# Performance work log

Hardware: AMD Instinct MI355X
Metric: run time of the kernel (lower is better)

Reference implementation:

```python
import jax, jax.numpy as jnp
import numpy as np

NUM_NODES = 100000
NUM_RELATIONS = 8
EMB_DIM = 128
HIDDEN_L = 64
NUM_LABELS = 32
NUM_EDGES = 1600000


def setup_inputs() -> dict:
    key = jax.random.key(0)
    ks = jax.random.split(key, 9)
    edge_index = jax.random.randint(ks[0], (2, NUM_EDGES), 0, NUM_NODES, dtype=jnp.int64)
    edge_type = jax.random.randint(ks[1], (NUM_EDGES,), 0, NUM_RELATIONS, dtype=jnp.int64)
    embedding = jax.random.normal(ks[2], (NUM_NODES, EMB_DIM), dtype=jnp.float32)
    W1 = jax.random.normal(ks[3], (NUM_RELATIONS, EMB_DIM, HIDDEN_L), dtype=jnp.float32) * (1.0 / np.sqrt(EMB_DIM))
    root1 = jax.random.normal(ks[4], (EMB_DIM, HIDDEN_L), dtype=jnp.float32) * (1.0 / np.sqrt(EMB_DIM))
    bias1 = jnp.zeros((HIDDEN_L,), dtype=jnp.float32)
    W2 = jax.random.normal(ks[5], (NUM_RELATIONS, HIDDEN_L, NUM_LABELS), dtype=jnp.float32) * (1.0 / np.sqrt(HIDDEN_L))
    root2 = jax.random.normal(ks[6], (HIDDEN_L, NUM_LABELS), dtype=jnp.float32) * (1.0 / np.sqrt(HIDDEN_L))
    bias2 = jnp.zeros((NUM_LABELS,), dtype=jnp.float32)
    return {"edge_index": edge_index, "edge_type": edge_type, "embedding": embedding,
            "W1": W1, "root1": root1, "bias1": bias1, "W2": W2, "root2": root2, "bias2": bias2}


def _rgcn_conv(x, edge_index, edge_type, W, root, bias):
    # PyG RGCNConv (default): out = bias + x @ root + sum_r mean_{j in N_r(i)} (x_j @ W_r)
    # Mean commutes with the linear map, so aggregate x_j per (dst, relation) first,
    # then apply the relation weights with one grouped einsum.
    n, r = x.shape[0], W.shape[0]
    src, dst = edge_index[0], edge_index[1]
    seg = dst * r + edge_type  # composite segment id: (node, relation)
    sums = jax.ops.segment_sum(x[src], seg, num_segments=n * r)          # [N*R, F_in]
    counts = jax.ops.segment_sum(jnp.ones_like(seg, dtype=x.dtype), seg, num_segments=n * r)
    mean = sums / jnp.maximum(counts, 1.0)[:, None]                      # [N*R, F_in]
    mean = mean.reshape(n, r, -1)                                        # [N, R, F_in]
    out = jnp.einsum('nrf,rfo->no', mean, W) + x @ root + bias           # [N, F_out]
    return out


def reference(edge_index, edge_type, embedding, W1, root1, bias1, W2, root2, bias2):
    x = _rgcn_conv(embedding, edge_index, edge_type, W1, root1, bias1)
    x = jax.nn.relu(x)
    x = _rgcn_conv(x, edge_index, edge_type, W2, root2, bias2)
    return jax.nn.sigmoid(x)
```

## Files before the change

kernel.cpp:

```cpp
#include <hip/hip_runtime.h>
#include <cstdint>

#define RR 8
#define D0 128
#define D1 64
#define D2 32
#define BINSH 8
#define EPB 4096

typedef unsigned short u16;
typedef unsigned int u32;
typedef short short8 __attribute__((ext_vector_type(8)));
typedef float floatx4 __attribute__((ext_vector_type(4)));

static __device__ __forceinline__ float relu_f(float x) { return x > 0.f ? x : 0.f; }
static __device__ __forceinline__ float sigm_f(float x) { return 1.0f / (1.0f + __expf(-x)); }

static __device__ __forceinline__ u16 f2bf(float x) {
  unsigned int u = __float_as_uint(x);
  u += 0x7fffu + ((u >> 16) & 1u);
  return (u16)(u >> 16);
}
static __device__ __forceinline__ float bf2f(u16 v) {
  return __uint_as_float(((unsigned int)v) << 16);
}

static __device__ __forceinline__ void packBTf_body(
    const float* __restrict__ W, const float* __restrict__ root,
    u16* __restrict__ BTf, int K, int NKf, int FOUT, int NC, int YC, int i) {
  if (i >= NC * K) return;
  int j = i & 7, l = (i >> 3) & 63, rest = i >> 9;
  int ks = rest % NKf, ct = rest / NKf;
  int c = ct * 16 + (l & 15);
  int k = ks * 32 + (l >> 4) * 8 + j;
  float v;
  if (c < YC) { int r = c / FOUT, o = c - r * FOUT; v = W[((size_t)r * K + k) * FOUT + o]; }
  else        { int o = c - YC; v = root[(size_t)k * (NC - YC) + o]; }
  BTf[i] = f2bf(v);
}

__global__ __launch_bounds__(256) void prep_k(
    const int* __restrict__ dstp, int E,
    const float* __restrict__ W1, const float* __restrict__ root1, u16* __restrict__ BT1,
    const float* __restrict__ W2, const float* __restrict__ root2, u16* __restrict__ BT2,
    int* __restrict__ histg, int NBIN, int NBLK, int nbBinA, int nbP1) {
  int b = blockIdx.x;
  if (b < nbBinA) {
    __shared__ int hist[512];
    int blk = b, t = threadIdx.x;
    for (int i = t; i < NBIN; i += 256) hist[i] = 0;
    __syncthreads();
    int base = blk * EPB + t;
#pragma unroll
    for (int j = 0; j < 16; ++j) {
      int e = base + j * 256;
      if (e < E) atomicAdd(&hist[dstp[e] >> BINSH], 1);
    }
    __syncthreads();
    for (int i = t; i < NBIN; i += 256) histg[(size_t)i * NBLK + blk] = hist[i];
  } else if (b < nbBinA + nbP1) {
    packBTf_body(W1, root1, BT1, D0, D0 / 32, D1, RR * D1 + D1, RR * D1,
                 (b - nbBinA) * 256 + threadIdx.x);
  } else {
    packBTf_body(W2, root2, BT2, D1, D1 / 32, D2, RR * D2 + D2, RR * D2,
                 (b - nbBinA - nbP1) * 256 + threadIdx.x);
  }
}

__global__ __launch_bounds__(256) void hsum_k(
    const int* __restrict__ histg, int* __restrict__ hbsum, int hl) {
  __shared__ int sd[256];
  int b = blockIdx.x, t = threadIdx.x;
  int base = b * 1024 + t * 4;
  int s = 0;
#pragma unroll
  for (int j = 0; j < 4; ++j) { int i = base + j; if (i < hl) s += histg[i]; }
  sd[t] = s; __syncthreads();
  for (int st = 128; st > 0; st >>= 1) { if (t < st) sd[t] += sd[t + st]; __syncthreads(); }
  if (t == 0) hbsum[b] = sd[0];
}

__global__ void hscan2_k(int* __restrict__ hbsum, int nb) {
  __shared__ int sd[256];
  int t = threadIdx.x;
  int v = (t < nb) ? hbsum[t] : 0;
  sd[t] = v; __syncthreads();
  for (int st = 1; st < 256; st <<= 1) {
    int x = (t >= st) ? sd[t - st] : 0;
    __syncthreads(); sd[t] += x; __syncthreads();
  }
  if (t < nb) hbsum[t] = sd[t] - v;
}

__global__ void hscan3_k(const int* __restrict__ histg, const int* __restrict__ hbsum,
                         int* __restrict__ hscan, int hl) {
  __shared__ int sd[256];
  int blk = blockIdx.x, t = threadIdx.x;
  int base = blk * 1024 + t * 4;
  int vals[4]; int s = 0; int loc[4];
#pragma unroll
  for (int j = 0; j < 4; ++j) {
    int i = base + j; int x = (i < hl) ? histg[i] : 0;
    vals[j] = x; loc[j] = s; s += x;
  }
  sd[t] = s; __syncthreads();
  for (int st = 1; st < 256; st <<= 1) {
    int x = (t >= st) ? sd[t - st] : 0;
    __syncthreads(); sd[t] += x; __syncthreads();
  }
  int texcl = sd[t] - s;
#pragma unroll
  for (int j = 0; j < 4; ++j) {
    int i = base + j;
    if (i < hl) {
      hscan[i] = hbsum[blk] + texcl + loc[j];
      if (i == hl - 1) hscan[hl] = hbsum[blk] + texcl + loc[j] + vals[j];
    }
  }
}

__global__ __launch_bounds__(256) void binB_k(
    const int* __restrict__ src, const int* __restrict__ dstp, const int* __restrict__ et,
    const int* __restrict__ hscan, int2* __restrict__ pk, int NBIN, int NBLK, int E) {
  __shared__ int curB[512];
  int blk = blockIdx.x, t = threadIdx.x;
  for (int i = t; i < NBIN; i += 256) curB[i] = hscan[(size_t)i * NBLK + blk];
  __syncthreads();
  int base = blk * EPB + t;
#pragma unroll
  for (int j = 0; j < 16; ++j) {
    int e = base + j * 256;
    if (e < E) {
      int d = dstp[e];
      int pos = atomicAdd(&curB[d >> BINSH], 1);
      pk[pos] = make_int2(src[e] * RR + et[e], d);
    }
  }
}

template <int K, int NC, int YC, bool AF32>
static __device__ __forceinline__ void gemm_body(
    const void* __restrict__ Aptr, const u16* __restrict__ BTf,
    const float* __restrict__ bias, u16* __restrict__ Y,
    float* __restrict__ Xroot, int N, int rowBlk, u16* __restrict__ smem) {
  constexpr int KP = K + 8;
  constexpr int NK = K / 32;
  constexpr int NCT = NC / 16;
  constexpr int ROOTC = NC - YC;
  constexpr int CH = K / 8;
  constexpr int YTS = 72;
  u16* const Al = smem;
  const int tid = threadIdx.x;

  if (AF32) {
    const float* A = (const float*)Aptr;
    for (int c = tid; c < 64 * CH; c += 256) {
      int row = c / CH, kc = c - row * CH;
      int gr = rowBlk * 64 + row; if (gr >= N) gr = N - 1;
      const float4* p = (const float4*)&A[(size_t)gr * K + kc * 8];
      float4 v0 = p[0], v1 = p[1];
      uint4 o;
      o.x = (u32)f2bf(v0.x) | ((u32)f2bf(v0.y) << 16);
      o.y = (u32)f2bf(v0.z) | ((u32)f2bf(v0.w) << 16);
      o.z = (u32)f2bf(v1.x) | ((u32)f2bf(v1.y) << 16);
      o.w = (u32)f2bf(v1.z) | ((u32)f2bf(v1.w) << 16);
      *(uint4*)&Al[row * KP + kc * 8] = o;
    }
  } else {
    const u16* A = (const u16*)Aptr;
    for (int c = tid; c < 64 * CH; c += 256) {
      int row = c / CH, kc = c - row * CH;
      int gr = rowBlk * 64 + row; if (gr >= N) gr = N - 1;
      *(uint4*)&Al[row * KP + kc * 8] = *(const uint4*)&A[(size_t)gr * K + kc * 8];
    }
  }
  __syncthreads();

  const int lane = tid & 63, wid = tid >> 6;
  const int l16 = lane & 15, quad = lane >> 4;
  const int wrow = (wid >> 1) * 32, wcol = (wid & 1) * 32;

  short8 af[2][NK];
#pragma unroll
  for (int ks = 0; ks < NK; ++ks) {
    int ko = ks * 32 + quad * 8;
    af[0][ks] = *(const short8*)&Al[(wrow +      l16) * KP + ko];
    af[1][ks] = *(const short8*)&Al[(wrow + 16 + l16) * KP + ko];
  }
  __syncthreads();

  int p = 0;
#pragma unroll
  for (int cb = 0; cb < NC; cb += 64, ++p) {
    int ct0 = (cb + wcol) >> 4; if (ct0 > NCT - 1) ct0 = NCT - 1;
    int ct1 = ct0 + 1;          if (ct1 > NCT - 1) ct1 = NCT - 1;

    short8 bf0[NK], bf1[NK];
#pragma unroll
    for (int ks = 0; ks < NK; ++ks) {
      bf0[ks] = *(const short8*)&BTf[((size_t)(ct0 * NK + ks) * 64 + lane) * 8];
      bf1[ks] = *(const short8*)&BTf[((size_t)(ct1 * NK + ks) * 64 + lane) * 8];
    }

    floatx4 acc[2][2] = {};
#pragma unroll
    for (int ks = 0; ks < NK; ++ks) {
      acc[0][0] = __builtin_amdgcn_mfma_f32_16x16x32_bf16(bf0[ks], af[0][ks], acc[0][0], 0, 0, 0);
      acc[0][1] = __builtin_amdgcn_mfma_f32_16x16x32_bf16(bf1[ks], af[0][ks], acc[0][1], 0, 0, 0);
      acc[1][0] = __builtin_amdgcn_mfma_f32_16x16x32_bf16(bf0[ks], af[1][ks], acc[1][0], 0, 0, 0);
      acc[1][1] = __builtin_amdgcn_mfma_f32_16x16x32_bf16(bf1[ks], af[1][ks], acc[1][1], 0, 0, 0);
    }

    if (cb + 64 <= YC) {
      u16* yt = smem + (p & 1) * (64 * YTS);
#pragma unroll
      for (int mi = 0; mi < 2; ++mi)
#pragma unroll
        for (int ni = 0; ni < 2; ++ni) {
          floatx4 v = acc[mi][ni];
          uint2 o;
          o.x = (u32)f2bf(v[0]) | ((u32)f2bf(v[1]) << 16);
          o.y = (u32)f2bf(v[2]) | ((u32)f2bf(v[3]) << 16);
          *(uint2*)&yt[(wrow + mi * 16 + l16) * YTS + wcol + ni * 16 + quad * 4] = o;
        }
    } else {
#pragma unroll
      for (int mi = 0; mi < 2; ++mi) {
        int r = rowBlk * 64 + wrow + mi * 16 + l16;
        if (r >= N) continue;
#pragma unroll
        for (int ni = 0; ni < 2; ++ni) {
          int cbase = cb + wcol + ni * 16 + quad * 4;
          floatx4 v = acc[mi][ni];
          if (cbase >= YC && cbase < NC) {
            int o = cbase - YC;
            float4 w;
            w.x = v[0] + bias[o];     w.y = v[1] + bias[o + 1];
            w.z = v[2] + bias[o + 2]; w.w = v[3] + bias[o + 3];
            *(float4*)&Xroot[(size_t)r * ROOTC + o] = w;
          }
        }
      }
    }
    __syncthreads();
    if (cb + 64 <= YC) {
      const u16* yt = smem + (p & 1) * (64 * YTS);
#pragma unroll
      for (int u = tid; u < 512; u += 256) {
        int row = u >> 3, cg = u & 7;
        int gr = rowBlk * 64 + row;
        if (gr < N)
          *(uint4*)&Y[(size_t)gr * YC + cb + cg * 8] = *(const uint4*)&yt[row * YTS + cg * 8];
      }
    }
  }
}

template <int K, int NC, int YC, bool AF32>
__global__ __launch_bounds__(256) void gemm_k(
    const void* __restrict__ Aptr, const u16* __restrict__ BTf,
    const float* __restrict__ bias, u16* __restrict__ Y,
    float* __restrict__ Xroot, int N) {
  constexpr int AL_U16 = 64 * (K + 8);
  constexpr int YT_U16 = 2 * 64 * 72;
  constexpr int SM_U16 = AL_U16 > YT_U16 ? AL_U16 : YT_U16;
  __shared__ __align__(16) u16 smem[SM_U16];
  gemm_body<K, NC, YC, AF32>(Aptr, BTf, bias, Y, Xroot, N, blockIdx.x, smem);
}

__global__ __launch_bounds__(256) void pgB2_k(
    const void* __restrict__ emb, const u16* __restrict__ BT1, const float* __restrict__ b1,
    u16* __restrict__ Y, float* __restrict__ xr1, int N, int nbBinC,
    const int2* __restrict__ pk, const int* __restrict__ hscan,
    int* __restrict__ offs, float* __restrict__ invc, int* __restrict__ ssr,
    int NBIN, int NBLK, int E) {
  constexpr int AL_U16 = 64 * (D0 + 8);
  constexpr int YT_U16 = 2 * 64 * 72;
  constexpr int SM_U16 = AL_U16 > YT_U16 ? AL_U16 : YT_U16;
  __shared__ __align__(16) u16 smem[SM_U16];
  if ((int)blockIdx.x >= nbBinC) {
    gemm_body<D0, RR * D1 + D1, RR * D1, true>(emb, BT1, b1, Y, xr1, N,
                                               blockIdx.x - nbBinC, smem);
    return;
  }
  int* cnt  = (int*)smem;
  int* tot  = cnt + 2048;
  int* sd   = tot + 256;
  int* curL = sd + 256;
  int b = blockIdx.x, t = threadIdx.x;
  int beg = hscan[(size_t)b * NBLK];
  int end = hscan[(size_t)(b + 1) * NBLK];
  int node0 = b << BINSH;

  for (int i = t; i < 2048; i += 256) cnt[i] = 0;
  __syncthreads();
  for (int i = beg + t; i < end; i += 256) {
    int2 p = pk[i];
    atomicAdd(&cnt[((p.y - node0) << 3) + (p.x & 7)], 1);
  }
  __syncthreads();

  int d = node0 + t;
  int s = 0;
  float iv[RR];
#pragma unroll
  for (int r = 0; r < RR; ++r) {
    int c = cnt[(t << 3) + r];
    s += c;
    iv[r] = 1.0f / (float)(c > 1 ? c : 1);
  }
  if (d < N) {
#pragma unroll
    for (int r = 0; r < RR; ++r) invc[(size_t)d * RR + r] = iv[r];
  }
  sd[t] = s; __syncthreads();
  for (int st = 1; st < 256; st <<= 1) {
    int x = (t >= st) ? sd[t - st] : 0;
    __syncthreads(); sd[t] += x; __syncthreads();
  }
  int excl = sd[t] - s;
  tot[t] = excl;
  if (d < N) offs[d] = beg + excl;
  if (d == N - 1) offs[N] = beg + excl + s;
  curL[t] = 0;
  __syncthreads();

  for (int i = beg + t; i < end; i += 256) {
    int2 p = pk[i];
    int ln = p.y - node0;
    int r = atomicAdd(&curL[ln], 1);
    ssr[beg + tot[ln] + r] = p.x;
  }
}

__global__ __launch_bounds__(256) void agg1_k(
    const int* __restrict__ off, const int* __restrict__ ssr,
    const uint4* __restrict__ Yu, const float* __restrict__ invc,
    const float4* __restrict__ xroot, uint4* __restrict__ X1b, int N, int E) {
  int d = blockIdx.x * 4 + (threadIdx.x >> 6);
  if (d >= N) return;
  int lane = threadIdx.x & 63;
  int h = lane >> 3, fi = lane & 7;
  int beg = off[d], end = off[d + 1];
  int deg = end - beg;
  int ei = beg + lane; if (ei >= E) ei = E - 1;
  int e = ssr[ei];
  float a0 = 0.f, a1 = 0.f, a2 = 0.f, a3 = 0.f, a4 = 0.f, a5 = 0.f, a6 = 0.f, a7 = 0.f;
  int dcap = deg < 64 ? deg : 64;
  for (int jb = 0; jb < dcap; jb += 16) {
    int j0 = jb + h, j1 = jb + 8 + h;
    int sr0 = __shfl(e, j0);
    int sr1 = __shfl(e, j1);
    if (j0 < deg) {
      float w = invc[(d << 3) + (sr0 & 7)];
      uint4 y = Yu[(size_t)sr0 * 8 + fi];
      a0 = fmaf(bf2f((u16)y.x), w, a0); a1 = fmaf(bf2f((u16)(y.x >> 16)), w, a1);
      a2 = fmaf(bf2f((u16)y.y), w, a2); a3 = fmaf(bf2f((u16)(y.y >> 16)), w, a3);
      a4 = fmaf(bf2f((u16)y.z), w, a4); a5 = fmaf(bf2f((u16)(y.z >> 16)), w, a5);
      a6 = fmaf(bf2f((u16)y.w), w, a6); a7 = fmaf(bf2f((u16)(y.w >> 16)), w, a7);
    }
    if (j1 < deg) {
      float w = invc[(d << 3) + (sr1 & 7)];
      uint4 y = Yu[(size_t)sr1 * 8 + fi];
      a0 = fmaf(bf2f((u16)y.x), w, a0); a1 = fmaf(bf2f((u16)(y.x >> 16)), w, a1);
      a2 = fmaf(bf2f((u16)y.y), w, a2); a3 = fmaf(bf2f((u16)(y.y >> 16)), w, a3);
      a4 = fmaf(bf2f((u16)y.z), w, a4); a5 = fmaf(bf2f((u16)(y.z >> 16)), w, a5);
      a6 = fmaf(bf2f((u16)y.w), w, a6); a7 = fmaf(bf2f((u16)(y.w >> 16)), w, a7);
    }
  }
  if (deg > 64) {
    for (int i = beg + 64 + h; i < end; i += 8) {
      int sr = ssr[i];
      float w = invc[(d << 3) + (sr & 7)];
      uint4 y = Yu[(size_t)sr * 8 + fi];
      a0 = fmaf(bf2f((u16)y.x), w, a0); a1 = fmaf(bf2f((u16)(y.x >> 16)), w, a1);
      a2 = fmaf(bf2f((u16)y.y), w, a2); a3 = fmaf(bf2f((u16)(y.y >> 16)), w, a3);
      a4 = fmaf(bf2f((u16)y.z), w, a4); a5 = fmaf(bf2f((u16)(y.z >> 16)), w, a5);
      a6 = fmaf(bf2f((u16)y.w), w, a6); a7 = fmaf(bf2f((u16)(y.w >> 16)), w, a7);
    }
  }
#pragma unroll
  for (int m = 32; m >= 8; m >>= 1) {
    a0 += __shfl_xor(a0, m); a1 += __shfl_xor(a1, m);
    a2 += __shfl_xor(a2, m); a3 += __shfl_xor(a3, m);
    a4 += __shfl_xor(a4, m); a5 += __shfl_xor(a5, m);
    a6 += __shfl_xor(a6, m); a7 += __shfl_xor(a7, m);
  }
  if (h == 0) {
    float4 xr0 = xroot[(size_t)d * 16 + fi * 2];
    float4 xr1 = xroot[(size_t)d * 16 + fi * 2 + 1];
    uint4 o;
    o.x = (u32)f2bf(relu_f(xr0.x + a0)) | ((u32)f2bf(relu_f(xr0.y + a1)) << 16);
    o.y = (u32)f2bf(relu_f(xr0.z + a2)) | ((u32)f2bf(relu_f(xr0.w + a3)) << 16);
    o.z = (u32)f2bf(relu_f(xr1.x + a4)) | ((u32)f2bf(relu_f(xr1.y + a5)) << 16);
    o.w = (u32)f2bf(relu_f(xr1.z + a6)) | ((u32)f2bf(relu_f(xr1.w + a7)) << 16);
    X1b[(size_t)d * 8 + fi] = o;
  }
}

__global__ __launch_bounds__(256) void agg2_k(
    const int* __restrict__ off, const int* __restrict__ ssr,
    const uint4* __restrict__ Yu, const float* __restrict__ invc,
    const float4* __restrict__ xroot, float4* __restrict__ out, int N, int E) {
  int d = blockIdx.x * 4 + (threadIdx.x >> 6);
  if (d >= N) return;
  int lane = threadIdx.x & 63;
  int h = lane >> 2, fi = lane & 3;
  int beg = off[d], end = off[d + 1];
  int deg = end - beg;
  int ei = beg + lane; if (ei >= E) ei = E - 1;
  int e = ssr[ei];
  float a0 = 0.f, a1 = 0.f, a2 = 0.f, a3 = 0.f, a4 = 0.f, a5 = 0.f, a6 = 0.f, a7 = 0.f;
  int dcap = deg < 64 ? deg : 64;
  for (int jb = 0; jb < dcap; jb += 32) {
    int j0 = jb + h, j1 = jb + 16 + h;
    int sr0 = __shfl(e, j0);
    int sr1 = __shfl(e, j1);
    if (j0 < deg) {
      float w = invc[(d << 3) + (sr0 & 7)];
      uint4 y = Yu[(size_t)sr0 * 4 + fi];
      a0 = fmaf(bf2f((u16)y.x), w, a0); a1 = fmaf(bf2f((u16)(y.x >> 16)), w, a1);
      a2 = fmaf(bf2f((u16)y.y), w, a2); a3 = fmaf(bf2f((u16)(y.y >> 16)), w, a3);
      a4 = fmaf(bf2f((u16)y.z), w, a4); a5 = fmaf(bf2f((u16)(y.z >> 16)), w, a5);
      a6 = fmaf(bf2f((u16)y.w), w, a6); a7 = fmaf(bf2f((u16)(y.w >> 16)), w, a7);
    }
    if (j1 < deg) {
      float w = invc[(d << 3) + (sr1 & 7)];
      uint4 y = Yu[(size_t)sr1 * 4 + fi];
      a0 = fmaf(bf2f((u16)y.x), w, a0); a1 = fmaf(bf2f((u16)(y.x >> 16)), w, a1);
      a2 = fmaf(bf2f((u16)y.y), w, a2); a3 = fmaf(bf2f((u16)(y.y >> 16)), w, a3);
      a4 = fmaf(bf2f((u16)y.z), w, a4); a5 = fmaf(bf2f((u16)(y.z >> 16)), w, a5);
      a6 = fmaf(bf2f((u16)y.w), w, a6); a7 = fmaf(bf2f((u16)(y.w >> 16)), w, a7);
    }
  }
  if (deg > 64) {
    for (int i = beg + 64 + h; i < end; i += 16) {
      int sr = ssr[i];
      float w = invc[(d << 3) + (sr & 7)];
      uint4 y = Yu[(size_t)sr * 4 + fi];
      a0 = fmaf(bf2f((u16)y.x), w, a0); a1 = fmaf(bf2f((u16)(y.x >> 16)), w, a1);
      a2 = fmaf(bf2f((u16)y.y), w, a2); a3 = fmaf(bf2f((u16)(y.y >> 16)), w, a3);
      a4 = fmaf(bf2f((u16)y.z), w, a4); a5 = fmaf(bf2f((u16)(y.z >> 16)), w, a5);
      a6 = fmaf(bf2f((u16)y.w), w, a6); a7 = fmaf(bf2f((u16)(y.w >> 16)), w, a7);
    }
  }
#pragma unroll
  for (int m = 32; m >= 4; m >>= 1) {
    a0 += __shfl_xor(a0, m); a1 += __shfl_xor(a1, m);
    a2 += __shfl_xor(a2, m); a3 += __shfl_xor(a3, m);
    a4 += __shfl_xor(a4, m); a5 += __shfl_xor(a5, m);
    a6 += __shfl_xor(a6, m); a7 += __shfl_xor(a7, m);
  }
  if (h == 0) {
    float4 xr0 = xroot[(size_t)d * 8 + fi * 2];
    float4 xr1 = xroot[(size_t)d * 8 + fi * 2 + 1];
    float4 o1, o2;
    o1.x = sigm_f(xr0.x + a0); o1.y = sigm_f(xr0.y + a1);
    o1.z = sigm_f(xr0.z + a2); o1.w = sigm_f(xr0.w + a3);
    o2.x = sigm_f(xr1.x + a4); o2.y = sigm_f(xr1.y + a5);
    o2.z = sigm_f(xr1.z + a6); o2.w = sigm_f(xr1.w + a7);
    out[(size_t)d * 8 + fi * 2]     = o1;
    out[(size_t)d * 8 + fi * 2 + 1] = o2;
  }
}

extern "C" void kernel_launch(void* const* d_in, const int* in_sizes, int n_in,
                              void* d_out, int out_size, void* d_ws, size_t ws_size,
                              hipStream_t stream) {
  const int*   edge_index = (const int*)d_in[0];
  const int*   et    = (const int*)d_in[1];
  const float* emb   = (const float*)d_in[2];
  const float* W1    = (const float*)d_in[3];
  const float* root1 = (const float*)d_in[4];
  const float* b1    = (const float*)d_in[5];
  const float* W2    = (const float*)d_in[6];
  const float* root2 = (const float*)d_in[7];
  const float* b2    = (const float*)d_in[8];
  float* out = (float*)d_out;

  const int E = in_sizes[1];
  const int N = in_sizes[2] / D0;
  const int* src  = edge_index;
  const int* dstp = edge_index + E;

  auto cdiv = [](size_t a, size_t b) { return (unsigned)((a + b - 1) / b); };

  const int NBLK = cdiv(E, EPB);
  const int NBIN = cdiv(N, 1 << BINSH);
  const int hl   = NBIN * NBLK;
  const int NHB  = cdiv(hl, 1024);

  char* ws = (char*)d_ws;
  size_t off_b = 0;
  auto alloc = [&](size_t bytes) { size_t o = off_b; off_b = (off_b + bytes + 255) & ~(size_t)255; return o; };
  float* invc   = (float*)(ws + alloc((size_t)N * RR * 4));
  int*   offs   = (int*)(ws + alloc((size_t)(N + 1) * 4));
  int*   hbsum  = (int*)(ws + alloc((size_t)256 * 4));
  int*   histg  = (int*)(ws + alloc((size_t)hl * 4));
  int*   hscan  = (int*)(ws + alloc((size_t)(hl + 1) * 4));
  int2*  pk     = (int2*)(ws + alloc((size_t)E * 8));
  int*   ssr    = (int*)(ws + alloc((size_t)E * 4));
  u16*   X1b    = (u16*)(ws + alloc((size_t)N * D1 * 2));
  float* xr1    = (float*)(ws + alloc((size_t)N * D1 * 4));
  float* xr2    = (float*)(ws + alloc((size_t)N * D2 * 4));
  u16*   BT1    = (u16*)(ws + alloc((size_t)(RR * D1 + D1) * D0 * 2));
  u16*   BT2    = (u16*)(ws + alloc((size_t)(RR * D2 + D2) * D1 * 2 + 8192));
  u16*   Y      = (u16*)(ws + alloc((size_t)N * RR * D1 * 2));

  const int NC1 = RR * D1 + D1;
  const int NC2 = RR * D2 + D2;
  const int nbP1 = cdiv((size_t)NC1 * D0, 256);
  const int nbP2 = cdiv((size_t)NC2 * D1, 256);
  const int nbGemm1 = cdiv(N, 64);

  prep_k<<<NBLK + nbP1 + nbP2, 256, 0, stream>>>(
      dstp, E, W1, root1, BT1, W2, root2, BT2, histg, NBIN, NBLK, NBLK, nbP1);
  hsum_k<<<NHB, 256, 0, stream>>>(histg, hbsum, hl);
  hscan2_k<<<1, 256, 0, stream>>>(hbsum, NHB);
  hscan3_k<<<NHB, 256, 0, stream>>>(histg, hbsum, hscan, hl);
  binB_k<<<NBLK, 256, 0, stream>>>(src, dstp, et, hscan, pk, NBIN, NBLK, E);
  pgB2_k<<<NBIN + nbGemm1, 256, 0, stream>>>(emb, BT1, b1, Y, xr1, N, NBIN,
                                             pk, hscan, offs, invc, ssr, NBIN, NBLK, E);
  agg1_k<<<cdiv(N, 4), 256, 0, stream>>>(offs, ssr, (const uint4*)Y, invc,
                                         (const float4*)xr1, (uint4*)X1b, N, E);
  gemm_k<D1, RR * D2 + D2, RR * D2, false><<<cdiv(N, 64), 256, 0, stream>>>(
      X1b, BT2, b2, Y, xr2, N);
  agg2_k<<<cdiv(N, 4), 256, 0, stream>>>(offs, ssr, (const uint4*)Y, invc,
                                         (const float4*)xr2, (float4*)out, N, E);
}
```

Before: 311.0 us.

## Write GEMM outputs directly from registers using permuted column layout

After: 318.5 us. 2.4% more time.

```diff
diff --git a/kernel.cpp b/kernel.cpp
--- a/kernel.cpp
+++ b/kernel.cpp
@@ -25,14 +25,19 @@
   return __uint_as_float(((unsigned int)v) << 16);
 }
 
+static __device__ __forceinline__ int perm64(int p) {
+  return (p & 32) | (((p >> 2) & 1) << 4) | (((p >> 3) & 3) << 2) | (p & 3);
+}
+
 static __device__ __forceinline__ void packBTf_body(
     const float* __restrict__ W, const float* __restrict__ root,
-    u16* __restrict__ BTf, int K, int NKf, int FOUT, int NC, int YC, int i) {
+    u16* __restrict__ BTf, int K, int NKf, int FOUT, int NC, int YC, bool PERM, int i) {
   if (i >= NC * K) return;
   int j = i & 7, l = (i >> 3) & 63, rest = i >> 9;
   int ks = rest % NKf, ct = rest / NKf;
   int c = ct * 16 + (l & 15);
   int k = ks * 32 + (l >> 4) * 8 + j;
+  if (PERM) k = perm64(k);
   float v;
   if (c < YC) { int r = c / FOUT, o = c - r * FOUT; v = W[((size_t)r * K + k) * FOUT + o]; }
   else        { int o = c - YC; v = root[(size_t)k * (NC - YC) + o]; }
@@ -59,10 +64,10 @@
     __syncthreads();
     for (int i = t; i < NBIN; i += 256) histg[(size_t)i * NBLK + blk] = hist[i];
   } else if (b < nbBinA + nbP1) {
-    packBTf_body(W1, root1, BT1, D0, D0 / 32, D1, RR * D1 + D1, RR * D1,
+    packBTf_body(W1, root1, BT1, D0, D0 / 32, D1, RR * D1 + D1, RR * D1, false,
                  (b - nbBinA) * 256 + threadIdx.x);
   } else {
-    packBTf_body(W2, root2, BT2, D1, D1 / 32, D2, RR * D2 + D2, RR * D2,
+    packBTf_body(W2, root2, BT2, D1, D1 / 32, D2, RR * D2 + D2, RR * D2, true,
                  (b - nbBinA - nbP1) * 256 + threadIdx.x);
   }
 }
@@ -148,7 +153,6 @@
   constexpr int NCT = NC / 16;
   constexpr int ROOTC = NC - YC;
   constexpr int CH = K / 8;
-  constexpr int YTS = 72;
   u16* const Al = smem;
   const int tid = threadIdx.x;
 
@@ -187,11 +191,9 @@
     af[0][ks] = *(const short8*)&Al[(wrow +      l16) * KP + ko];
     af[1][ks] = *(const short8*)&Al[(wrow + 16 + l16) * KP + ko];
   }
-  __syncthreads();
-
-  int p = 0;
-#pragma unroll
-  for (int cb = 0; cb < NC; cb += 64, ++p) {
+
+#pragma unroll
+  for (int cb = 0; cb < NC; cb += 64) {
     int ct0 = (cb + wcol) >> 4; if (ct0 > NCT - 1) ct0 = NCT - 1;
     int ct1 = ct0 + 1;          if (ct1 > NCT - 1) ct1 = NCT - 1;
 
@@ -212,17 +214,17 @@
     }
 
     if (cb + 64 <= YC) {
-      u16* yt = smem + (p & 1) * (64 * YTS);
-#pragma unroll
-      for (int mi = 0; mi < 2; ++mi)
-#pragma unroll
-        for (int ni = 0; ni < 2; ++ni) {
-          floatx4 v = acc[mi][ni];
-          uint2 o;
-          o.x = (u32)f2bf(v[0]) | ((u32)f2bf(v[1]) << 16);
-          o.y = (u32)f2bf(v[2]) | ((u32)f2bf(v[3]) << 16);
-          *(uint2*)&yt[(wrow + mi * 16 + l16) * YTS + wcol + ni * 16 + quad * 4] = o;
-        }
+#pragma unroll
+      for (int mi = 0; mi < 2; ++mi) {
+        int r = rowBlk * 64 + wrow + mi * 16 + l16;
+        if (r >= N) continue;
+        uint4 o;
+        o.x = (u32)f2bf(acc[mi][0][0]) | ((u32)f2bf(acc[mi][0][1]) << 16);
+        o.y = (u32)f2bf(acc[mi][0][2]) | ((u32)f2bf(acc[mi][0][3]) << 16);
+        o.z = (u32)f2bf(acc[mi][1][0]) | ((u32)f2bf(acc[mi][1][1]) << 16);
+        o.w = (u32)f2bf(acc[mi][1][2]) | ((u32)f2bf(acc[mi][1][3]) << 16);
+        *(uint4*)&Y[(size_t)r * YC + cb + wcol + quad * 8] = o;
+      }
     } else {
 #pragma unroll
       for (int mi = 0; mi < 2; ++mi) {
@@ -233,24 +235,14 @@
           int cbase = cb + wcol + ni * 16 + quad * 4;
           floatx4 v = acc[mi][ni];
           if (cbase >= YC && cbase < NC) {
-            int o = cbase - YC;
+            int oc = cbase - YC;
+            int op = wcol + quad * 8 + ni * 4;
             float4 w;
-            w.x = v[0] + bias[o];     w.y = v[1] + bias[o + 1];
-            w.z = v[2] + bias[o + 2]; w.w = v[3] + bias[o + 3];
-            *(float4*)&Xroot[(size_t)r * ROOTC + o] = w;
+            w.x = v[0] + bias[oc];     w.y = v[1] + bias[oc + 1];
+            w.z = v[2] + bias[oc + 2]; w.w = v[3] + bias[oc + 3];
+            *(float4*)&Xroot[(size_t)r * ROOTC + op] = w;
           }
         }
-      }
-    }
-    __syncthreads();
-    if (cb + 64 <= YC) {
-      const u16* yt = smem + (p & 1) * (64 * YTS);
-#pragma unroll
-      for (int u = tid; u < 512; u += 256) {
-        int row = u >> 3, cg = u & 7;
-        int gr = rowBlk * 64 + row;
-        if (gr < N)
-          *(uint4*)&Y[(size_t)gr * YC + cb + cg * 8] = *(const uint4*)&yt[row * YTS + cg * 8];
       }
     }
   }
@@ -261,10 +253,7 @@
     const void* __restrict__ Aptr, const u16* __restrict__ BTf,
     const float* __restrict__ bias, u16* __restrict__ Y,
     float* __restrict__ Xroot, int N) {
-  constexpr int AL_U16 = 64 * (K + 8);
-  constexpr int YT_U16 = 2 * 64 * 72;
-  constexpr int SM_U16 = AL_U16 > YT_U16 ? AL_U16 : YT_U16;
-  __shared__ __align__(16) u16 smem[SM_U16];
+  __shared__ __align__(16) u16 smem[64 * (K + 8)];
   gemm_body<K, NC, YC, AF32>(Aptr, BTf, bias, Y, Xroot, N, blockIdx.x, smem);
 }
 
@@ -274,10 +263,7 @@
     const int2* __restrict__ pk, const int* __restrict__ hscan,
     int* __restrict__ offs, float* __restrict__ invc, int* __restrict__ ssr,
     int NBIN, int NBLK, int E) {
-  constexpr int AL_U16 = 64 * (D0 + 8);
-  constexpr int YT_U16 = 2 * 64 * 72;
-  constexpr int SM_U16 = AL_U16 > YT_U16 ? AL_U16 : YT_U16;
-  __shared__ __align__(16) u16 smem[SM_U16];
+  __shared__ __align__(16) u16 smem[64 * (D0 + 8)];
   if ((int)blockIdx.x >= nbBinC) {
     gemm_body<D0, RR * D1 + D1, RR * D1, true>(emb, BT1, b1, Y, xr1, N,
                                                blockIdx.x - nbBinC, smem);
@@ -401,7 +387,7 @@
 __global__ __launch_bounds__(256) void agg2_k(
     const int* __restrict__ off, const int* __restrict__ ssr,
     const uint4* __restrict__ Yu, const float* __restrict__ invc,
-    const float4* __restrict__ xroot, float4* __restrict__ out, int N, int E) {
+    const float4* __restrict__ xroot, float* __restrict__ out, int N, int E) {
   int d = blockIdx.x * 4 + (threadIdx.x >> 6);
   if (d >= N) return;
   int lane = threadIdx.x & 63;
@@ -459,8 +445,8 @@
     o1.z = sigm_f(xr0.z + a2); o1.w = sigm_f(xr0.w + a3);
     o2.x = sigm_f(xr1.x + a4); o2.y = sigm_f(xr1.y + a5);
     o2.z = sigm_f(xr1.z + a6); o2.w = sigm_f(xr1.w + a7);
-    out[(size_t)d * 8 + fi * 2]     = o1;
-    out[(size_t)d * 8 + fi * 2 + 1] = o2;
+    *(float4*)&out[(size_t)d * 32 + fi * 4]      = o1;
+    *(float4*)&out[(size_t)d * 32 + 16 + fi * 4] = o2;
   }
 }
 
@@ -526,5 +512,5 @@
   gemm_k<D1, RR * D2 + D2, RR * D2, false><<<cdiv(N, 64), 256, 0, stream>>>(
       X1b, BT2, b2, Y, xr2, N);
   agg2_k<<<cdiv(N, 4), 256, 0, stream>>>(offs, ssr, (const uint4*)Y, invc,
-                                         (const float4*)xr2, (float4*)out, N, E);
-}
+                                         (const float4*)xr2, out, N, E);
+}
```

## Fuse layer-1 aggregation with layer-2 GEMM in one kernel via LDS tile

Applied to the files above, without the earlier changes.

Result: slower. 335.6 us (+7.9%).

```diff
diff --git a/kernel.cpp b/kernel.cpp
--- a/kernel.cpp
+++ b/kernel.cpp
@@ -254,18 +254,6 @@
       }
     }
   }
-}
-
-template <int K, int NC, int YC, bool AF32>
-__global__ __launch_bounds__(256) void gemm_k(
-    const void* __restrict__ Aptr, const u16* __restrict__ BTf,
-    const float* __restrict__ bias, u16* __restrict__ Y,
-    float* __restrict__ Xroot, int N) {
-  constexpr int AL_U16 = 64 * (K + 8);
-  constexpr int YT_U16 = 2 * 64 * 72;
-  constexpr int SM_U16 = AL_U16 > YT_U16 ? AL_U16 : YT_U16;
-  __shared__ __align__(16) u16 smem[SM_U16];
-  gemm_body<K, NC, YC, AF32>(Aptr, BTf, bias, Y, Xroot, N, blockIdx.x, smem);
 }
 
 __global__ __launch_bounds__(256) void pgB2_k(
@@ -333,68 +321,166 @@
   }
 }
 
-__global__ __launch_bounds__(256) void agg1_k(
+__global__ __launch_bounds__(256) void agg1g_k(
     const int* __restrict__ off, const int* __restrict__ ssr,
     const uint4* __restrict__ Yu, const float* __restrict__ invc,
-    const float4* __restrict__ xroot, uint4* __restrict__ X1b, int N, int E) {
-  int d = blockIdx.x * 4 + (threadIdx.x >> 6);
-  if (d >= N) return;
-  int lane = threadIdx.x & 63;
-  int h = lane >> 3, fi = lane & 7;
-  int beg = off[d], end = off[d + 1];
-  int deg = end - beg;
-  int ei = beg + lane; if (ei >= E) ei = E - 1;
-  int e = ssr[ei];
-  float a0 = 0.f, a1 = 0.f, a2 = 0.f, a3 = 0.f, a4 = 0.f, a5 = 0.f, a6 = 0.f, a7 = 0.f;
-  int dcap = deg < 64 ? deg : 64;
-  for (int jb = 0; jb < dcap; jb += 16) {
-    int j0 = jb + h, j1 = jb + 8 + h;
-    int sr0 = __shfl(e, j0);
-    int sr1 = __shfl(e, j1);
-    if (j0 < deg) {
-      float w = invc[(d << 3) + (sr0 & 7)];
-      uint4 y = Yu[(size_t)sr0 * 8 + fi];
-      a0 = fmaf(bf2f((u16)y.x), w, a0); a1 = fmaf(bf2f((u16)(y.x >> 16)), w, a1);
-      a2 = fmaf(bf2f((u16)y.y), w, a2); a3 = fmaf(bf2f((u16)(y.y >> 16)), w, a3);
-      a4 = fmaf(bf2f((u16)y.z), w, a4); a5 = fmaf(bf2f((u16)(y.z >> 16)), w, a5);
-      a6 = fmaf(bf2f((u16)y.w), w, a6); a7 = fmaf(bf2f((u16)(y.w >> 16)), w, a7);
-    }
-    if (j1 < deg) {
-      float w = invc[(d << 3) + (sr1 & 7)];
-      uint4 y = Yu[(size_t)sr1 * 8 + fi];
-      a0 = fmaf(bf2f((u16)y.x), w, a0); a1 = fmaf(bf2f((u16)(y.x >> 16)), w, a1);
-      a2 = fmaf(bf2f((u16)y.y), w, a2); a3 = fmaf(bf2f((u16)(y.y >> 16)), w, a3);
-      a4 = fmaf(bf2f((u16)y.z), w, a4); a5 = fmaf(bf2f((u16)(y.z >> 16)), w, a5);
-      a6 = fmaf(bf2f((u16)y.w), w, a6); a7 = fmaf(bf2f((u16)(y.w >> 16)), w, a7);
-    }
-  }
-  if (deg > 64) {
-    for (int i = beg + 64 + h; i < end; i += 8) {
-      int sr = ssr[i];
-      float w = invc[(d << 3) + (sr & 7)];
-      uint4 y = Yu[(size_t)sr * 8 + fi];
-      a0 = fmaf(bf2f((u16)y.x), w, a0); a1 = fmaf(bf2f((u16)(y.x >> 16)), w, a1);
-      a2 = fmaf(bf2f((u16)y.y), w, a2); a3 = fmaf(bf2f((u16)(y.y >> 16)), w, a3);
-      a4 = fmaf(bf2f((u16)y.z), w, a4); a5 = fmaf(bf2f((u16)(y.z >> 16)), w, a5);
-      a6 = fmaf(bf2f((u16)y.w), w, a6); a7 = fmaf(bf2f((u16)(y.w >> 16)), w, a7);
-    }
-  }
-#pragma unroll
-  for (int m = 32; m >= 8; m >>= 1) {
-    a0 += __shfl_xor(a0, m); a1 += __shfl_xor(a1, m);
-    a2 += __shfl_xor(a2, m); a3 += __shfl_xor(a3, m);
-    a4 += __shfl_xor(a4, m); a5 += __shfl_xor(a5, m);
-    a6 += __shfl_xor(a6, m); a7 += __shfl_xor(a7, m);
-  }
-  if (h == 0) {
-    float4 xr0 = xroot[(size_t)d * 16 + fi * 2];
-    float4 xr1 = xroot[(size_t)d * 16 + fi * 2 + 1];
-    uint4 o;
-    o.x = (u32)f2bf(relu_f(xr0.x + a0)) | ((u32)f2bf(relu_f(xr0.y + a1)) << 16);
-    o.y = (u32)f2bf(relu_f(xr0.z + a2)) | ((u32)f2bf(relu_f(xr0.w + a3)) << 16);
-    o.z = (u32)f2bf(relu_f(xr1.x + a4)) | ((u32)f2bf(relu_f(xr1.y + a5)) << 16);
-    o.w = (u32)f2bf(relu_f(xr1.z + a6)) | ((u32)f2bf(relu_f(xr1.w + a7)) << 16);
-    X1b[(size_t)d * 8 + fi] = o;
+    const float4* __restrict__ xroot, const u16* __restrict__ BT2f,
+    const float* __restrict__ b2, u16* __restrict__ Y2,
+    float* __restrict__ xr2, int N, int E) {
+  constexpr int NK = D1 / 32;
+  constexpr int NC = RR * D2 + D2;
+  constexpr int YC = RR * D2;
+  constexpr int NCT = NC / 16;
+  constexpr int ROOTC = D2;
+  constexpr int TS = 72;
+  __shared__ __align__(16) u16 smem[2 * 64 * TS];
+  u16* const At = smem;
+  const int tid = threadIdx.x;
+  const int wid = tid >> 6, lane = tid & 63;
+  const int h = lane >> 3, fi = lane & 7;
+  const int dbase = (int)blockIdx.x * 64;
+
+  for (int i = 0; i < 16; ++i) {
+    int dl = wid * 16 + i;
+    int d = dbase + dl;
+    if (d < N) {
+      int beg = off[d], end = off[d + 1];
+      int deg = end - beg;
+      int ei = beg + lane; if (ei >= E) ei = E - 1;
+      int e = ssr[ei];
+      float a0 = 0.f, a1 = 0.f, a2 = 0.f, a3 = 0.f, a4 = 0.f, a5 = 0.f, a6 = 0.f, a7 = 0.f;
+      int dcap = deg < 64 ? deg : 64;
+      for (int jb = 0; jb < dcap; jb += 16) {
+        int j0 = jb + h, j1 = jb + 8 + h;
+        int sr0 = __shfl(e, j0);
+        int sr1 = __shfl(e, j1);
+        if (j0 < deg) {
+          float w = invc[(d << 3) + (sr0 & 7)];
+          uint4 y = Yu[(size_t)sr0 * 8 + fi];
+          a0 = fmaf(bf2f((u16)y.x), w, a0); a1 = fmaf(bf2f((u16)(y.x >> 16)), w, a1);
+          a2 = fmaf(bf2f((u16)y.y), w, a2); a3 = fmaf(bf2f((u16)(y.y >> 16)), w, a3);
+          a4 = fmaf(bf2f((u16)y.z), w, a4); a5 = fmaf(bf2f((u16)(y.z >> 16)), w, a5);
+          a6 = fmaf(bf2f((u16)y.w), w, a6); a7 = fmaf(bf2f((u16)(y.w >> 16)), w, a7);
+        }
+        if (j1 < deg) {
+          float w = invc[(d << 3) + (sr1 & 7)];
+          uint4 y = Yu[(size_t)sr1 * 8 + fi];
+          a0 = fmaf(bf2f((u16)y.x), w, a0); a1 = fmaf(bf2f((u16)(y.x >> 16)), w, a1);
+          a2 = fmaf(bf2f((u16)y.y), w, a2); a3 = fmaf(bf2f((u16)(y.y >> 16)), w, a3);
+          a4 = fmaf(bf2f((u16)y.z), w, a4); a5 = fmaf(bf2f((u16)(y.z >> 16)), w, a5);
+          a6 = fmaf(bf2f((u16)y.w), w, a6); a7 = fmaf(bf2f((u16)(y.w >> 16)), w, a7);
+        }
+      }
+      if (deg > 64) {
+        for (int ii = beg + 64 + h; ii < end; ii += 8) {
+          int sr = ssr[ii];
+          float w = invc[(d << 3) + (sr & 7)];
+          uint4 y = Yu[(size_t)sr * 8 + fi];
+          a0 = fmaf(bf2f((u16)y.x), w, a0); a1 = fmaf(bf2f((u16)(y.x >> 16)), w, a1);
+          a2 = fmaf(bf2f((u16)y.y), w, a2); a3 = fmaf(bf2f((u16)(y.y >> 16)), w, a3);
+          a4 = fmaf(bf2f((u16)y.z), w, a4); a5 = fmaf(bf2f((u16)(y.z >> 16)), w, a5);
+          a6 = fmaf(bf2f((u16)y.w), w, a6); a7 = fmaf(bf2f((u16)(y.w >> 16)), w, a7);
+        }
+      }
+#pragma unroll
+      for (int m = 32; m >= 8; m >>= 1) {
+        a0 += __shfl_xor(a0, m); a1 += __shfl_xor(a1, m);
+        a2 += __shfl_xor(a2, m); a3 += __shfl_xor(a3, m);
+        a4 += __shfl_xor(a4, m); a5 += __shfl_xor(a5, m);
+        a6 += __shfl_xor(a6, m); a7 += __shfl_xor(a7, m);
+      }
+      if (h == 0) {
+        float4 xr0 = xroot[(size_t)d * 16 + fi * 2];
+        float4 xr1v = xroot[(size_t)d * 16 + fi * 2 + 1];
+        uint4 o;
+        o.x = (u32)f2bf(relu_f(xr0.x + a0)) | ((u32)f2bf(relu_f(xr0.y + a1)) << 16);
+        o.y = (u32)f2bf(relu_f(xr0.z + a2)) | ((u32)f2bf(relu_f(xr0.w + a3)) << 16);
+        o.z = (u32)f2bf(relu_f(xr1v.x + a4)) | ((u32)f2bf(relu_f(xr1v.y + a5)) << 16);
+        o.w = (u32)f2bf(relu_f(xr1v.z + a6)) | ((u32)f2bf(relu_f(xr1v.w + a7)) << 16);
+        *(uint4*)&At[dl * TS + fi * 8] = o;
+      }
+    } else {
+      if (h == 0) *(uint4*)&At[dl * TS + fi * 8] = make_uint4(0, 0, 0, 0);
+    }
+  }
+  __syncthreads();
+
+  const int l16 = lane & 15, quad = lane >> 4;
+  const int wrow = (wid >> 1) * 32, wcol = (wid & 1) * 32;
+
+  short8 af[2][NK];
+#pragma unroll
+  for (int ks = 0; ks < NK; ++ks) {
+    int ko = ks * 32 + quad * 8;
+    af[0][ks] = *(const short8*)&At[(wrow +      l16) * TS + ko];
+    af[1][ks] = *(const short8*)&At[(wrow + 16 + l16) * TS + ko];
+  }
+  __syncthreads();
+
+  int p = 0;
+#pragma unroll
+  for (int cb = 0; cb < NC; cb += 64, ++p) {
+    int ct0 = (cb + wcol) >> 4; if (ct0 > NCT - 1) ct0 = NCT - 1;
+    int ct1 = ct0 + 1;          if (ct1 > NCT - 1) ct1 = NCT - 1;
+
+    short8 bf0[NK], bf1[NK];
+#pragma unroll
+    for (int ks = 0; ks < NK; ++ks) {
+      bf0[ks] = *(const short8*)&BT2f[((size_t)(ct0 * NK + ks) * 64 + lane) * 8];
+      bf1[ks] = *(const short8*)&BT2f[((size_t)(ct1 * NK + ks) * 64 + lane) * 8];
+    }
+
+    floatx4 acc[2][2] = {};
+#pragma unroll
+    for (int ks = 0; ks < NK; ++ks) {
+      acc[0][0] = __builtin_amdgcn_mfma_f32_16x16x32_bf16(bf0[ks], af[0][ks], acc[0][0], 0, 0, 0);
+      acc[0][1] = __builtin_amdgcn_mfma_f32_16x16x32_bf16(bf1[ks], af[0][ks], acc[0][1], 0, 0, 0);
+      acc[1][0] = __builtin_amdgcn_mfma_f32_16x16x32_bf16(bf0[ks], af[1][ks], acc[1][0], 0, 0, 0);
+      acc[1][1] = __builtin_amdgcn_mfma_f32_16x16x32_bf16(bf1[ks], af[1][ks], acc[1][1], 0, 0, 0);
+    }
+
+    if (cb + 64 <= YC) {
+      u16* yt = smem + (p & 1) * (64 * TS);
+#pragma unroll
+      for (int mi = 0; mi < 2; ++mi)
+#pragma unroll
+        for (int ni = 0; ni < 2; ++ni) {
+          floatx4 v = acc[mi][ni];
+          uint2 o;
+          o.x = (u32)f2bf(v[0]) | ((u32)f2bf(v[1]) << 16);
+          o.y = (u32)f2bf(v[2]) | ((u32)f2bf(v[3]) << 16);
+          *(uint2*)&yt[(wrow + mi * 16 + l16) * TS + wcol + ni * 16 + quad * 4] = o;
+        }
+    } else {
+#pragma unroll
+      for (int mi = 0; mi < 2; ++mi) {
+        int r = dbase + wrow + mi * 16 + l16;
+        if (r >= N) continue;
+#pragma unroll
+        for (int ni = 0; ni < 2; ++ni) {
+          int cbase = cb + wcol + ni * 16 + quad * 4;
+          floatx4 v = acc[mi][ni];
+          if (cbase >= YC && cbase < NC) {
+            int o = cbase - YC;
+            float4 w;
+            w.x = v[0] + b2[o];     w.y = v[1] + b2[o + 1];
+            w.z = v[2] + b2[o + 2]; w.w = v[3] + b2[o + 3];
+            *(float4*)&xr2[(size_t)r * ROOTC + o] = w;
+          }
+        }
+      }
+    }
+    __syncthreads();
+    if (cb + 64 <= YC) {
+      const u16* yt = smem + (p & 1) * (64 * TS);
+#pragma unroll
+      for (int u = tid; u < 512; u += 256) {
+        int row = u >> 3, cg = u & 7;
+        int gr = dbase + row;
+        if (gr < N)
+          *(uint4*)&Y2[(size_t)gr * YC + cb + cg * 8] = *(const uint4*)&yt[row * TS + cg * 8];
+      }
+    }
   }
 }
 
@@ -500,12 +586,12 @@
   int*   hscan  = (int*)(ws + alloc((size_t)(hl + 1) * 4));
   int2*  pk     = (int2*)(ws + alloc((size_t)E * 8));
   int*   ssr    = (int*)(ws + alloc((size_t)E * 4));
-  u16*   X1b    = (u16*)(ws + alloc((size_t)N * D1 * 2));
   float* xr1    = (float*)(ws + alloc((size_t)N * D1 * 4));
   float* xr2    = (float*)(ws + alloc((size_t)N * D2 * 4));
   u16*   BT1    = (u16*)(ws + alloc((size_t)(RR * D1 + D1) * D0 * 2));
   u16*   BT2    = (u16*)(ws + alloc((size_t)(RR * D2 + D2) * D1 * 2 + 8192));
   u16*   Y      = (u16*)(ws + alloc((size_t)N * RR * D1 * 2));
+  u16*   Y2     = (u16*)(ws + alloc((size_t)N * RR * D2 * 2));
 
   const int NC1 = RR * D1 + D1;
   const int NC2 = RR * D2 + D2;
@@ -521,10 +607,8 @@
   binB_k<<<NBLK, 256, 0, stream>>>(src, dstp, et, hscan, pk, NBIN, NBLK, E);
   pgB2_k<<<NBIN + nbGemm1, 256, 0, stream>>>(emb, BT1, b1, Y, xr1, N, NBIN,
                                              pk, hscan, offs, invc, ssr, NBIN, NBLK, E);
-  agg1_k<<<cdiv(N, 4), 256, 0, stream>>>(offs, ssr, (const uint4*)Y, invc,
-                                         (const float4*)xr1, (uint4*)X1b, N, E);
-  gemm_k<D1, RR * D2 + D2, RR * D2, false><<<cdiv(N, 64), 256, 0, stream>>>(
-      X1b, BT2, b2, Y, xr2, N);
-  agg2_k<<<cdiv(N, 4), 256, 0, stream>>>(offs, ssr, (const uint4*)Y, invc,
+  agg1g_k<<<cdiv(N, 64), 256, 0, stream>>>(offs, ssr, (const uint4*)Y, invc,
+                                           (const float4*)xr1, BT2, b2, Y2, xr2, N, E);
+  agg2_k<<<cdiv(N, 4), 256, 0, stream>>>(offs, ssr, (const uint4*)Y2, invc,
                                          (const float4*)xr2, (float4*)out, N, E);
 }
```

## Pack multiple destination nodes per wavefront in aggregation and fuse scan kernels

Applied to the files above, without the earlier changes.

Result: faster. 297.6 us (-4.3%).

```diff
diff --git a/kernel.cpp b/kernel.cpp
--- a/kernel.cpp
+++ b/kernel.cpp
@@ -80,29 +80,28 @@
   if (t == 0) hbsum[b] = sd[0];
 }
 
-__global__ void hscan2_k(int* __restrict__ hbsum, int nb) {
+__global__ void hscan3_k(const int* __restrict__ histg, const int* __restrict__ hbsum,
+                         int* __restrict__ hscan, int hl, int nhb) {
   __shared__ int sd[256];
-  int t = threadIdx.x;
-  int v = (t < nb) ? hbsum[t] : 0;
+  __shared__ int sbase;
+  int blk = blockIdx.x, t = threadIdx.x;
+  int v = (t < nhb) ? hbsum[t] : 0;
   sd[t] = v; __syncthreads();
   for (int st = 1; st < 256; st <<= 1) {
     int x = (t >= st) ? sd[t - st] : 0;
     __syncthreads(); sd[t] += x; __syncthreads();
   }
-  if (t < nb) hbsum[t] = sd[t] - v;
-}
-
-__global__ void hscan3_k(const int* __restrict__ histg, const int* __restrict__ hbsum,
-                         int* __restrict__ hscan, int hl) {
-  __shared__ int sd[256];
-  int blk = blockIdx.x, t = threadIdx.x;
-  int base = blk * 1024 + t * 4;
+  if (t == 0) sbase = (blk == 0) ? 0 : sd[blk - 1];
+  __syncthreads();
+  int base = sbase;
+  int cb = blk * 1024 + t * 4;
   int vals[4]; int s = 0; int loc[4];
 #pragma unroll
   for (int j = 0; j < 4; ++j) {
-    int i = base + j; int x = (i < hl) ? histg[i] : 0;
+    int i = cb + j; int x = (i < hl) ? histg[i] : 0;
     vals[j] = x; loc[j] = s; s += x;
   }
+  __syncthreads();
   sd[t] = s; __syncthreads();
   for (int st = 1; st < 256; st <<= 1) {
     int x = (t >= st) ? sd[t - st] : 0;
@@ -111,10 +110,10 @@
   int texcl = sd[t] - s;
 #pragma unroll
   for (int j = 0; j < 4; ++j) {
-    int i = base + j;
+    int i = cb + j;
     if (i < hl) {
-      hscan[i] = hbsum[blk] + texcl + loc[j];
-      if (i == hl - 1) hscan[hl] = hbsum[blk] + texcl + loc[j] + vals[j];
+      hscan[i] = base + texcl + loc[j];
+      if (i == hl - 1) hscan[hl] = base + texcl + loc[j] + vals[j];
     }
   }
 }
@@ -337,56 +336,51 @@
     const int* __restrict__ off, const int* __restrict__ ssr,
     const uint4* __restrict__ Yu, const float* __restrict__ invc,
     const float4* __restrict__ xroot, uint4* __restrict__ X1b, int N, int E) {
-  int d = blockIdx.x * 4 + (threadIdx.x >> 6);
-  if (d >= N) return;
-  int lane = threadIdx.x & 63;
-  int h = lane >> 3, fi = lane & 7;
-  int beg = off[d], end = off[d + 1];
+  int wid = threadIdx.x >> 6, lane = threadIdx.x & 63;
+  int half = lane >> 5, l32 = lane & 31;
+  int h = l32 >> 3, fi = l32 & 7;
+  int d = blockIdx.x * 8 + wid * 2 + half;
+  bool act = d < N;
+  int beg = 0, end = 0;
+  if (act) { beg = off[d]; end = off[d + 1]; }
   int deg = end - beg;
-  int ei = beg + lane; if (ei >= E) ei = E - 1;
+  int ei = beg + l32; if (ei >= E) ei = E - 1;
   int e = ssr[ei];
   float a0 = 0.f, a1 = 0.f, a2 = 0.f, a3 = 0.f, a4 = 0.f, a5 = 0.f, a6 = 0.f, a7 = 0.f;
-  int dcap = deg < 64 ? deg : 64;
+#define ACC1(s) { \
+    float w = invc[(d << 3) + ((s) & 7)]; \
+    uint4 y = Yu[(size_t)(s) * 8 + fi]; \
+    a0 = fmaf(bf2f((u16)y.x), w, a0); a1 = fmaf(bf2f((u16)(y.x >> 16)), w, a1); \
+    a2 = fmaf(bf2f((u16)y.y), w, a2); a3 = fmaf(bf2f((u16)(y.y >> 16)), w, a3); \
+    a4 = fmaf(bf2f((u16)y.z), w, a4); a5 = fmaf(bf2f((u16)(y.z >> 16)), w, a5); \
+    a6 = fmaf(bf2f((u16)y.w), w, a6); a7 = fmaf(bf2f((u16)(y.w >> 16)), w, a7); }
+  int dcap = deg < 32 ? deg : 32;
   for (int jb = 0; jb < dcap; jb += 16) {
-    int j0 = jb + h, j1 = jb + 8 + h;
-    int sr0 = __shfl(e, j0);
-    int sr1 = __shfl(e, j1);
-    if (j0 < deg) {
-      float w = invc[(d << 3) + (sr0 & 7)];
-      uint4 y = Yu[(size_t)sr0 * 8 + fi];
-      a0 = fmaf(bf2f((u16)y.x), w, a0); a1 = fmaf(bf2f((u16)(y.x >> 16)), w, a1);
-      a2 = fmaf(bf2f((u16)y.y), w, a2); a3 = fmaf(bf2f((u16)(y.y >> 16)), w, a3);
-      a4 = fmaf(bf2f((u16)y.z), w, a4); a5 = fmaf(bf2f((u16)(y.z >> 16)), w, a5);
-      a6 = fmaf(bf2f((u16)y.w), w, a6); a7 = fmaf(bf2f((u16)(y.w >> 16)), w, a7);
-    }
-    if (j1 < deg) {
-      float w = invc[(d << 3) + (sr1 & 7)];
-      uint4 y = Yu[(size_t)sr1 * 8 + fi];
-      a0 = fmaf(bf2f((u16)y.x), w, a0); a1 = fmaf(bf2f((u16)(y.x >> 16)), w, a1);
-      a2 = fmaf(bf2f((u16)y.y), w, a2); a3 = fmaf(bf2f((u16)(y.y >> 16)), w, a3);
-      a4 = fmaf(bf2f((u16)y.z), w, a4); a5 = fmaf(bf2f((u16)(y.z >> 16)), w, a5);
-      a6 = fmaf(bf2f((u16)y.w), w, a6); a7 = fmaf(bf2f((u16)(y.w >> 16)), w, a7);
-    }
-  }
-  if (deg > 64) {
-    for (int i = beg + 64 + h; i < end; i += 8) {
+    int j0 = jb + h, j1 = jb + 4 + h, j2 = jb + 8 + h, j3 = jb + 12 + h;
+    int s0 = __shfl(e, half * 32 + j0);
+    int s1 = __shfl(e, half * 32 + j1);
+    int s2 = __shfl(e, half * 32 + j2);
+    int s3 = __shfl(e, half * 32 + j3);
+    if (j0 < deg) ACC1(s0)
+    if (j1 < deg) ACC1(s1)
+    if (j2 < deg) ACC1(s2)
+    if (j3 < deg) ACC1(s3)
+  }
+  if (deg > 32) {
+    for (int i = beg + 32 + h; i < end; i += 4) {
       int sr = ssr[i];
-      float w = invc[(d << 3) + (sr & 7)];
-      uint4 y = Yu[(size_t)sr * 8 + fi];
-      a0 = fmaf(bf2f((u16)y.x), w, a0); a1 = fmaf(bf2f((u16)(y.x >> 16)), w, a1);
-      a2 = fmaf(bf2f((u16)y.y), w, a2); a3 = fmaf(bf2f((u16)(y.y >> 16)), w, a3);
-      a4 = fmaf(bf2f((u16)y.z), w, a4); a5 = fmaf(bf2f((u16)(y.z >> 16)), w, a5);
-      a6 = fmaf(bf2f((u16)y.w), w, a6); a7 = fmaf(bf2f((u16)(y.w >> 16)), w, a7);
-    }
-  }
-#pragma unroll
-  for (int m = 32; m >= 8; m >>= 1) {
+      ACC1(sr)
+    }
+  }
+#undef ACC1
+#pragma unroll
+  for (int m = 16; m >= 8; m >>= 1) {
     a0 += __shfl_xor(a0, m); a1 += __shfl_xor(a1, m);
     a2 += __shfl_xor(a2, m); a3 += __shfl_xor(a3, m);
     a4 += __shfl_xor(a4, m); a5 += __shfl_xor(a5, m);
     a6 += __shfl_xor(a6, m); a7 += __shfl_xor(a7, m);
   }
-  if (h == 0) {
+  if (act && h == 0) {
     float4 xr0 = xroot[(size_t)d * 16 + fi * 2];
     float4 xr1 = xroot[(size_t)d * 16 + fi * 2 + 1];
     uint4 o;
@@ -402,56 +396,51 @@
     const int* __restrict__ off, const int* __restrict__ ssr,
     const uint4* __restrict__ Yu, const float* __restrict__ invc,
     const float4* __restrict__ xroot, float4* __restrict__ out, int N, int E) {
-  int d = blockIdx.x * 4 + (threadIdx.x >> 6);
-  if (d >= N) return;
-  int lane = threadIdx.x & 63;
-  int h = lane >> 2, fi = lane & 3;
-  int beg = off[d], end = off[d + 1];
+  int wid = threadIdx.x >> 6, lane = threadIdx.x & 63;
+  int q = lane >> 4, l16 = lane & 15;
+  int h = l16 >> 2, fi = l16 & 3;
+  int d = blockIdx.x * 16 + wid * 4 + q;
+  bool act = d < N;
+  int beg = 0, end = 0;
+  if (act) { beg = off[d]; end = off[d + 1]; }
   int deg = end - beg;
-  int ei = beg + lane; if (ei >= E) ei = E - 1;
+  int ei = beg + l16; if (ei >= E) ei = E - 1;
   int e = ssr[ei];
   float a0 = 0.f, a1 = 0.f, a2 = 0.f, a3 = 0.f, a4 = 0.f, a5 = 0.f, a6 = 0.f, a7 = 0.f;
-  int dcap = deg < 64 ? deg : 64;
-  for (int jb = 0; jb < dcap; jb += 32) {
-    int j0 = jb + h, j1 = jb + 16 + h;
-    int sr0 = __shfl(e, j0);
-    int sr1 = __shfl(e, j1);
-    if (j0 < deg) {
-      float w = invc[(d << 3) + (sr0 & 7)];
-      uint4 y = Yu[(size_t)sr0 * 4 + fi];
-      a0 = fmaf(bf2f((u16)y.x), w, a0); a1 = fmaf(bf2f((u16)(y.x >> 16)), w, a1);
-      a2 = fmaf(bf2f((u16)y.y), w, a2); a3 = fmaf(bf2f((u16)(y.y >> 16)), w, a3);
-      a4 = fmaf(bf2f((u16)y.z), w, a4); a5 = fmaf(bf2f((u16)(y.z >> 16)), w, a5);
-      a6 = fmaf(bf2f((u16)y.w), w, a6); a7 = fmaf(bf2f((u16)(y.w >> 16)), w, a7);
-    }
-    if (j1 < deg) {
-      float w = invc[(d << 3) + (sr1 & 7)];
-      uint4 y = Yu[(size_t)sr1 * 4 + fi];
-      a0 = fmaf(bf2f((u16)y.x), w, a0); a1 = fmaf(bf2f((u16)(y.x >> 16)), w, a1);
-      a2 = fmaf(bf2f((u16)y.y), w, a2); a3 = fmaf(bf2f((u16)(y.y >> 16)), w, a3);
-      a4 = fmaf(bf2f((u16)y.z), w, a4); a5 = fmaf(bf2f((u16)(y.z >> 16)), w, a5);
-      a6 = fmaf(bf2f((u16)y.w), w, a6); a7 = fmaf(bf2f((u16)(y.w >> 16)), w, a7);
-    }
-  }
-  if (deg > 64) {
-    for (int i = beg + 64 + h; i < end; i += 16) {
+#define ACC2(s) { \
+    float w = invc[(d << 3) + ((s) & 7)]; \
+    uint4 y = Yu[(size_t)(s) * 4 + fi]; \
+    a0 = fmaf(bf2f((u16)y.x), w, a0); a1 = fmaf(bf2f((u16)(y.x >> 16)), w, a1); \
+    a2 = fmaf(bf2f((u16)y.y), w, a2); a3 = fmaf(bf2f((u16)(y.y >> 16)), w, a3); \
+    a4 = fmaf(bf2f((u16)y.z), w, a4); a5 = fmaf(bf2f((u16)(y.z >> 16)), w, a5); \
+    a6 = fmaf(bf2f((u16)y.w), w, a6); a7 = fmaf(bf2f((u16)(y.w >> 16)), w, a7); }
+  int dcap = deg < 16 ? deg : 16;
+  for (int jb = 0; jb < dcap; jb += 16) {
+    int j0 = jb + h, j1 = jb + 4 + h, j2 = jb + 8 + h, j3 = jb + 12 + h;
+    int s0 = __shfl(e, q * 16 + j0);
+    int s1 = __shfl(e, q * 16 + j1);
+    int s2 = __shfl(e, q * 16 + j2);
+    int s3 = __shfl(e, q * 16 + j3);
+    if (j0 < deg) ACC2(s0)
+    if (j1 < deg) ACC2(s1)
+    if (j2 < deg) ACC2(s2)
+    if (j3 < deg) ACC2(s3)
+  }
+  if (deg > 16) {
+    for (int i = beg + 16 + h; i < end; i += 4) {
       int sr = ssr[i];
-      float w = invc[(d << 3) + (sr & 7)];
-      uint4 y = Yu[(size_t)sr * 4 + fi];
-      a0 = fmaf(bf2f((u16)y.x), w, a0); a1 = fmaf(bf2f((u16)(y.x >> 16)), w, a1);
-      a2 = fmaf(bf2f((u16)y.y), w, a2); a3 = fmaf(bf2f((u16)(y.y >> 16)), w, a3);
-      a4 = fmaf(bf2f((u16)y.z), w, a4); a5 = fmaf(bf2f((u16)(y.z >> 16)), w, a5);
-      a6 = fmaf(bf2f((u16)y.w), w, a6); a7 = fmaf(bf2f((u16)(y.w >> 16)), w, a7);
-    }
-  }
-#pragma unroll
-  for (int m = 32; m >= 4; m >>= 1) {
+      ACC2(sr)
+    }
+  }
+#undef ACC2
+#pragma unroll
+  for (int m = 8; m >= 4; m >>= 1) {
     a0 += __shfl_xor(a0, m); a1 += __shfl_xor(a1, m);
     a2 += __shfl_xor(a2, m); a3 += __shfl_xor(a3, m);
     a4 += __shfl_xor(a4, m); a5 += __shfl_xor(a5, m);
     a6 += __shfl_xor(a6, m); a7 += __shfl_xor(a7, m);
   }
-  if (h == 0) {
+  if (act && h == 0) {
     float4 xr0 = xroot[(size_t)d * 8 + fi * 2];
     float4 xr1 = xroot[(size_t)d * 8 + fi * 2 + 1];
     float4 o1, o2;
@@ -516,15 +505,14 @@
   prep_k<<<NBLK + nbP1 + nbP2, 256, 0, stream>>>(
       dstp, E, W1, root1, BT1, W2, root2, BT2, histg, NBIN, NBLK, NBLK, nbP1);
   hsum_k<<<NHB, 256, 0, stream>>>(histg, hbsum, hl);
-  hscan2_k<<<1, 256, 0, stream>>>(hbsum, NHB);
-  hscan3_k<<<NHB, 256, 0, stream>>>(histg, hbsum, hscan, hl);
+  hscan3_k<<<NHB, 256, 0, stream>>>(histg, hbsum, hscan, hl, NHB);
   binB_k<<<NBLK, 256, 0, stream>>>(src, dstp, et, hscan, pk, NBIN, NBLK, E);
   pgB2_k<<<NBIN + nbGemm1, 256, 0, stream>>>(emb, BT1, b1, Y, xr1, N, NBIN,
                                              pk, hscan, offs, invc, ssr, NBIN, NBLK, E);
-  agg1_k<<<cdiv(N, 4), 256, 0, stream>>>(offs, ssr, (const uint4*)Y, invc,
+  agg1_k<<<cdiv(N, 8), 256, 0, stream>>>(offs, ssr, (const uint4*)Y, invc,
                                          (const float4*)xr1, (uint4*)X1b, N, E);
   gemm_k<D1, RR * D2 + D2, RR * D2, false><<<cdiv(N, 64), 256, 0, stream>>>(
       X1b, BT2, b2, Y, xr2, N);
-  agg2_k<<<cdiv(N, 4), 256, 0, stream>>>(offs, ssr, (const uint4*)Y, invc,
-                                         (const float4*)xr2, (float4*)out, N, E);
-}
+  agg2_k<<<cdiv(N, 16), 256, 0, stream>>>(offs, ssr, (const uint4*)Y, invc,
+                                          (const float4*)xr2, (float4*)out, N, E);
+}
```
